# Optimization experiments

Hardware: AMD Instinct MI355X
Metric: run time of the kernel (lower is better)

The kernel has to match this reference:

```python
import jax, jax.numpy as jnp
import numpy as np

N_NODES = 20000
N_EDGES = 320000
EMB = 128


def setup_inputs() -> dict:
    key = jax.random.key(0)
    ks = jax.random.split(key, 8)
    h = jax.random.normal(ks[0], (N_NODES, EMB), dtype=jnp.float32)
    W1 = jax.random.normal(ks[1], (2 * EMB, 4 * EMB), dtype=jnp.float32) / np.sqrt(2 * EMB)
    b1 = jnp.zeros((4 * EMB,), dtype=jnp.float32)
    W2 = jax.random.normal(ks[2], (4 * EMB, 1), dtype=jnp.float32) / np.sqrt(4 * EMB)
    b2 = jnp.zeros((1,), dtype=jnp.float32)
    # logistic-noise uniforms for RelaxedBernoulli rsample, kept away from {0,1}
    u = jax.random.uniform(ks[3], (N_EDGES,), dtype=jnp.float32, minval=1e-6, maxval=1.0 - 1e-6)
    row = jax.random.randint(ks[4], (N_EDGES,), 0, N_NODES, dtype=jnp.int32)
    col = jax.random.randint(ks[5], (N_EDGES,), 0, N_NODES, dtype=jnp.int32)
    edge_mask = -jnp.ones((N_EDGES,), dtype=jnp.int32)  # torch code initializes mask to -1
    return {"h": h, "W1": W1, "b1": b1, "W2": W2, "b2": b2,
            "u": u, "row": row, "col": col, "edge_mask": edge_mask, "hierarchy": 0}


def _segment_softmax(scores, seg, num_segments):
    m = jax.ops.segment_max(scores, seg, num_segments=num_segments)
    e = jnp.exp(scores - m[seg])
    s = jax.ops.segment_sum(e, seg, num_segments=num_segments)
    return e / s[seg]


TEMPERATURE = 1.0
RATIO = 0.5  # threshold for hard bernoulli


def reference(h, W1, b1, W2, b2, u, row, col, edge_mask, hierarchy):
    # edge gather + concat: [E, 2*EMB]
    edge_rep = jnp.concatenate([h[row], h[col]], axis=-1)
    # 2-layer MLP edge scorer -> [E]
    hid = jax.nn.relu(edge_rep @ W1 + b1)
    scores = (hid @ W2 + b2).reshape(-1)
    # segment softmax over edges grouped by source node (torch: softmax(edge_score, edge_index[0]))
    probs = _segment_softmax(scores, row, N_NODES)
    # RelaxedBernoulli(temperature, probs).rsample(): sigmoid((logits + logistic)/T)
    logits = jnp.log(probs) - jnp.log1p(-probs)
    logistic = jnp.log(u) - jnp.log1p(-u)
    y = jax.nn.sigmoid((logits + logistic) / TEMPERATURE)
    y_hard = (y > RATIO).astype(y.dtype)
    y_st = jax.lax.stop_gradient(y_hard - y) + y  # straight-through
    # edge_mask[y == 1] = hierarchy + 1
    new_mask = jnp.where(y_st == 1.0, jnp.int32(hierarchy + 1), edge_mask)
    c_idx = new_mask > 0
    s_idx = new_mask == -1
    causal_w = jnp.where(c_idx, scores, 0.0)
    spu_w = jnp.where(s_idx, -scores, 0.0)
    return scores, y_st, new_mask, causal_w, spu_w
```

## Files before the change

### kernel.cpp

```cpp
#include <hip/hip_runtime.h>
#include <math.h>

#define N_NODES 20000
#define N_EDGES 320000
#define EMB 128
#define HID 512
#define NCHUNK ((N_NODES + 1023) / 1024)

#define RPW 4
#define WPB 2
#define RPB (RPW * WPB)
#define FE_BLOCKS ((N_NODES + RPB - 1) / RPB)

#define GEMM_MT ((N_NODES + 127) / 128)
#define GEMM_MFMA_BLOCKS (GEMM_MT * 8)
#define HIST_BLOCKS ((N_EDGES + 255) / 256)
#define GH_BLOCKS (GEMM_MFMA_BLOCKS + HIST_BLOCKS)
#define N_HTILES (N_NODES / 16)

#define PREP_H_BLOCKS 2500
#define PREP_W_BLOCKS 512
#define PREP_BLOCKS (PREP_H_BLOCKS + PREP_W_BLOCKS)

typedef __attribute__((ext_vector_type(8))) short bf16x8;
typedef __attribute__((ext_vector_type(4))) float f32x4;

#define MFMA16(a, b, c) __builtin_amdgcn_mfma_f32_16x16x32_bf16((a), (b), (c), 0, 0, 0)

__global__ void init_deg(int* __restrict__ deg, int* __restrict__ offs) {
    int i = blockIdx.x * 256 + threadIdx.x;
    if (i < N_NODES) deg[i] = 0;
    if (i == 0) offs[N_NODES] = N_EDGES;
}

__device__ __forceinline__ unsigned short bf16rn(float x) {
    unsigned u = __builtin_bit_cast(unsigned, x);
    u += 0x7FFFu + ((u >> 16) & 1u);
    return (unsigned short)(u >> 16);
}
__device__ __forceinline__ float bf2f(unsigned short b) {
    unsigned u = ((unsigned)b) << 16;
    return __builtin_bit_cast(float, u);
}
__device__ __forceinline__ void split3(float x, unsigned short& s1,
                                       unsigned short& s2, unsigned short& s3) {
    s1 = bf16rn(x);
    float r = x - bf2f(s1);
    s2 = bf16rn(r);
    float r2 = r - bf2f(s2);
    s3 = bf16rn(r2);
}

__global__ __launch_bounds__(256) void prep_pack(
    const float* __restrict__ h, const float* __restrict__ W1,
    unsigned short* __restrict__ hp1, unsigned short* __restrict__ hp2,
    unsigned short* __restrict__ hp3,
    unsigned short* __restrict__ wp1, unsigned short* __restrict__ wp2,
    unsigned short* __restrict__ wp3)
{
    const int bid = blockIdx.x, tid = threadIdx.x;

    if (bid < PREP_H_BLOCKS) {
        const int i4 = bid * 256 + tid;
        const float4 v = ((const float4*)h)[i4];
        const int r  = i4 >> 5;
        const int k0 = (i4 & 31) << 2;
        const int t = r >> 4, rowi = r & 15;
        const int ks = k0 >> 5;
        const int ln = (((k0 >> 3) & 3) << 4) + rowi;
        const int j0 = k0 & 7;
        const size_t off = (size_t)((t * 4 + ks) * 512) + ln * 8 + j0;
        unsigned short a1[4], a2[4], a3[4];
        split3(v.x, a1[0], a2[0], a3[0]);
        split3(v.y, a1[1], a2[1], a3[1]);
        split3(v.z, a1[2], a2[2], a3[2]);
        split3(v.w, a1[3], a2[3], a3[3]);
#define PACK4(dst, a) { \
            uint2 pk; \
            pk.x = (unsigned)a[0] | ((unsigned)a[1] << 16); \
            pk.y = (unsigned)a[2] | ((unsigned)a[3] << 16); \
            *(uint2*)((dst) + off) = pk; }
        PACK4(hp1, a1); PACK4(hp2, a2); PACK4(hp3, a3);
#undef PACK4
        return;
    }

    const int t = (bid - PREP_H_BLOCKS) * 256 + tid;
    const int n = t & 1023, k = t >> 10;
    const float x = W1[(size_t)(((n >> 9) << 7) + k) * HID + (n & 511)];
    unsigned short s1, s2, s3;
    split3(x, s1, s2, s3);
    const int tn = n >> 4, rown = n & 15;
    const int ks = k >> 5;
    const int ln = (((k >> 3) & 3) << 4) + rown;
    const int j = k & 7;
    const size_t off = (size_t)((tn * 4 + ks) * 512) + ln * 8 + j;
    wp1[off] = s1; wp2[off] = s2; wp3[off] = s3;
}

__global__ __launch_bounds__(256) void gemm_mfma(
    const unsigned short* __restrict__ hp1, const unsigned short* __restrict__ hp2,
    const unsigned short* __restrict__ hp3,
    const unsigned short* __restrict__ wp1, const unsigned short* __restrict__ wp2,
    const unsigned short* __restrict__ wp3,
    const float* __restrict__ b1, float* __restrict__ P, float* __restrict__ Q,
    const int* __restrict__ row, int* __restrict__ deg)
{
    const int bid = blockIdx.x;
    const int tid = threadIdx.x;

    if (bid >= GEMM_MFMA_BLOCKS) {
        const int e = (bid - GEMM_MFMA_BLOCKS) * 256 + tid;
        if (e < N_EDGES) atomicAdd(&deg[row[e]], 1);
        return;
    }

    const int nt = bid & 7, mt = bid >> 3;
    const int lane = tid & 63, w = tid >> 6;
    const int wm = w >> 1, wn = w & 1;
    const int l15 = lane & 15, l4 = lane >> 4;

    int tA[4];
#pragma unroll
    for (int i = 0; i < 4; ++i) {
        int t = mt * 8 + wm * 4 + i;
        tA[i] = (t < N_HTILES) ? t : N_HTILES - 1;
    }
    const int tB0 = nt * 8 + wn * 4;

    f32x4 acc[4][4];
#pragma unroll
    for (int i = 0; i < 4; ++i)
#pragma unroll
        for (int j = 0; j < 4; ++j) acc[i][j] = (f32x4){0.f, 0.f, 0.f, 0.f};

    const size_t lo = (size_t)lane * 8;

#pragma unroll
    for (int ks = 0; ks < 4; ++ks) {
        bf16x8 A1[4], A2[4], A3[4];
#pragma unroll
        for (int i = 0; i < 4; ++i) {
            const size_t ao = (size_t)((tA[i] * 4 + ks) * 512) + lo;
            A1[i] = *(const bf16x8*)(hp1 + ao);
            A2[i] = *(const bf16x8*)(hp2 + ao);
            A3[i] = *(const bf16x8*)(hp3 + ao);
        }
        const size_t b_base = (size_t)((tB0 * 4 + ks) * 512) + lo;
        bf16x8 Ba1 = *(const bf16x8*)(wp1 + b_base);
        bf16x8 Ba2 = *(const bf16x8*)(wp2 + b_base);
        bf16x8 Ba3 = *(const bf16x8*)(wp3 + b_base);
#pragma unroll
        for (int jn = 0; jn < 4; ++jn) {
            bf16x8 Bn1, Bn2, Bn3;
            if (jn < 3) {
                const size_t bo = b_base + (size_t)(jn + 1) * 2048;
                Bn1 = *(const bf16x8*)(wp1 + bo);
                Bn2 = *(const bf16x8*)(wp2 + bo);
                Bn3 = *(const bf16x8*)(wp3 + bo);
            }
#pragma unroll
            for (int i = 0; i < 4; ++i) {
                acc[i][jn] = MFMA16(A1[i], Ba1, acc[i][jn]);
                acc[i][jn] = MFMA16(A1[i], Ba2, acc[i][jn]);
                acc[i][jn] = MFMA16(A2[i], Ba1, acc[i][jn]);
                acc[i][jn] = MFMA16(A2[i], Ba2, acc[i][jn]);
                acc[i][jn] = MFMA16(A1[i], Ba3, acc[i][jn]);
                acc[i][jn] = MFMA16(A3[i], Ba1, acc[i][jn]);
            }
            if (jn < 3) { Ba1 = Bn1; Ba2 = Bn2; Ba3 = Bn3; }
        }
    }

    const int rbase = mt * 128 + wm * 64 + l4 * 4;
#pragma unroll
    for (int jn = 0; jn < 4; ++jn) {
        const int n = nt * 128 + wn * 64 + jn * 16 + l15;
        const bool isP = n < 512;
        float* __restrict__ dst = isP ? P : Q;
        const int col = n & 511;
        const float bias = isP ? b1[col] : 0.0f;
#pragma unroll
        for (int i = 0; i < 4; ++i) {
            const int rr0 = rbase + i * 16;
#pragma unroll
            for (int r = 0; r < 4; ++r) {
                const int rr = rr0 + r;
                if (rr < N_NODES)
                    dst[(size_t)rr * HID + col] = acc[i][jn][r] + bias;
            }
        }
    }
}

__device__ __forceinline__ int wave_incl_scan(int v, int lane) {
#pragma unroll
    for (int off = 1; off < 64; off <<= 1) {
        int t = __shfl_up(v, off, 64);
        if (lane >= off) v += t;
    }
    return v;
}

__global__ __launch_bounds__(1024) void scan_part(const int* __restrict__ deg,
                                                  int* __restrict__ part,
                                                  int* __restrict__ totals) {
    __shared__ int wsum[16];
    const int tid = threadIdx.x, lane = tid & 63, w = tid >> 6;
    const int i = blockIdx.x * 1024 + tid;
    int v = (i < N_NODES) ? deg[i] : 0;
    int incl = wave_incl_scan(v, lane);
    if (lane == 63) wsum[w] = incl;
    __syncthreads();
    if (w == 0) {
        int x = (lane < 16) ? wsum[lane] : 0;
        int xs = wave_incl_scan(x, lane);
        if (lane < 16) wsum[lane] = xs - x;
        if (lane == 15) totals[blockIdx.x] = xs;
    }
    __syncthreads();
    if (i < N_NODES) part[i] = wsum[w] + incl - v;
}

__global__ __launch_bounds__(1024) void scan_apply(const int* __restrict__ part,
                                                   const int* __restrict__ totals,
                                                   int* __restrict__ cursor,
                                                   int* __restrict__ offs) {
    __shared__ int carry_s;
    const int tid = threadIdx.x;
    if (tid < 64) {
        int v = (tid < NCHUNK) ? totals[tid] : 0;
        int incl = wave_incl_scan(v, tid);
        if (tid == (int)blockIdx.x) carry_s = incl - v;
    }
    __syncthreads();
    const int i = blockIdx.x * 1024 + tid;
    if (i < N_NODES) {
        int o = part[i] + carry_s;
        cursor[i] = o;
        offs[i] = o;
    }
}

__global__ void scatter_edges(const int* __restrict__ row, const int* __restrict__ col,
                              int* __restrict__ cursor,
                              unsigned short* __restrict__ cols16,
                              int* __restrict__ inv) {
    int e = blockIdx.x * 256 + threadIdx.x;
    if (e >= N_EDGES) return;
    int r = row[e];
    int pos = atomicAdd(&cursor[r], 1);
    cols16[pos] = (unsigned short)col[e];
    inv[e] = pos;
}

__device__ __forceinline__ float dot8_relu(const float4 qa, const float4 qb,
                                           const float4 p0, const float4 p1,
                                           const float4 w0, const float4 w1) {
    float t = 0.0f;
    t = fmaf(fmaxf(p0.x + qa.x, 0.0f), w0.x, t);
    t = fmaf(fmaxf(p0.y + qa.y, 0.0f), w0.y, t);
    t = fmaf(fmaxf(p0.z + qa.z, 0.0f), w0.z, t);
    t = fmaf(fmaxf(p0.w + qa.w, 0.0f), w0.w, t);
    t = fmaf(fmaxf(p1.x + qb.x, 0.0f), w1.x, t);
    t = fmaf(fmaxf(p1.y + qb.y, 0.0f), w1.y, t);
    t = fmaf(fmaxf(p1.z + qb.z, 0.0f), w1.z, t);
    t = fmaf(fmaxf(p1.w + qb.w, 0.0f), w1.w, t);
    return t;
}

__device__ __forceinline__ float chunk_scores(
    const float* __restrict__ Q, const unsigned short* __restrict__ cols16,
    int es_base, int nch, int lane, int j0,
    const float4 p0, const float4 p1, const float4 w0, const float4 w1,
    float bias2)
{
    int mycol = 0;
    if (lane < nch) mycol = (int)cols16[es_base + lane];
    float mysc = -INFINITY;

#define QL2(k, bb, d0, d1) { \
        int c_ = __shfl(mycol, (bb) + (k), 64); \
        const float* __restrict__ q_ = Q + (size_t)c_ * HID; \
        d0 = *(const float4*)(q_ + j0); \
        d1 = *(const float4*)(q_ + 256 + j0); }

    float4 a00, a01, a10, a11;
    QL2(0, 0, a00, a01); QL2(1, 0, a10, a11);

    for (int b = 0; b < nch; b += 2) {
        float4 n00, n01, n10, n11;
        const bool more = (b + 2) < nch;
        if (more) { QL2(0, b + 2, n00, n01); QL2(1, b + 2, n10, n11); }

        float s0 = dot8_relu(a00, a01, p0, p1, w0, w1);
        float s1 = dot8_relu(a10, a11, p0, p1, w0, w1);

#pragma unroll
        for (int off = 32; off > 0; off >>= 1) {
            s0 += __shfl_xor(s0, off, 64);
            s1 += __shfl_xor(s1, off, 64);
        }

        const int k = lane - b;
        if ((unsigned)k < 2u && lane < nch) mysc = (k ? s1 : s0) + bias2;

        if (more) { a00 = n00; a01 = n01; a10 = n10; a11 = n11; }
    }
#undef QL2
    return mysc;
}

__global__ __launch_bounds__(128) void fused_edge(
    const float* __restrict__ P, const float* __restrict__ Q,
    const float* __restrict__ W2, const float* __restrict__ b2,
    const unsigned short* __restrict__ cols16, const int* __restrict__ offs,
    float2* __restrict__ tmp)
{
    const int tid = threadIdx.x, lane = tid & 63, w = tid >> 6;
    const int r0 = blockIdx.x * RPB + w * RPW;
    const int r1 = (r0 + RPW < N_NODES) ? r0 + RPW : N_NODES;
    const int j0 = lane << 2;

    const float4 w0 = *(const float4*)(W2 + j0);
    const float4 w1 = *(const float4*)(W2 + 256 + j0);
    const float bias2 = b2[0];

    for (int r = r0; r < r1; ++r) {
        const int es = offs[r], ee = offs[r + 1];
        const int d = ee - es;
        if (d == 0) continue;

        const float* __restrict__ prow = P + (size_t)r * HID;
        const float4 p0 = *(const float4*)(prow + j0);
        const float4 p1 = *(const float4*)(prow + 256 + j0);

        if (d <= 64) {
            float mysc = chunk_scores(Q, cols16, es, d, lane, j0,
                                      p0, p1, w0, w1, bias2);

            float m = mysc;
#pragma unroll
            for (int off = 32; off > 0; off >>= 1)
                m = fmaxf(m, __shfl_xor(m, off, 64));

            float ev = (lane < d) ? expf(mysc - m) : 0.0f;
            float ssum = ev;
#pragma unroll
            for (int off = 32; off > 0; off >>= 1)
                ssum += __shfl_xor(ssum, off, 64);

            if (lane < d) {
                float p = ev / ssum;
                float logits = logf(p) - log1pf(-p);
                tmp[es + lane] = make_float2(mysc, logits);
            }
        } else {
            for (int base = 0; base < d; base += 64) {
                const int nch = (d - base < 64) ? d - base : 64;
                float mysc = chunk_scores(Q, cols16, es + base, nch, lane, j0,
                                          p0, p1, w0, w1, bias2);
                if (lane < nch) tmp[es + base + lane].x = mysc;
            }

            float m = -INFINITY;
            for (int j = lane; j < d; j += 64)
                m = fmaxf(m, tmp[es + j].x);
#pragma unroll
            for (int off = 32; off > 0; off >>= 1)
                m = fmaxf(m, __shfl_xor(m, off, 64));

            float ssum = 0.0f;
            for (int j = lane; j < d; j += 64)
                ssum += expf(tmp[es + j].x - m);
#pragma unroll
            for (int off = 32; off > 0; off >>= 1)
                ssum += __shfl_xor(ssum, off, 64);

            for (int j = lane; j < d; j += 64) {
                float s = tmp[es + j].x;
                float p = expf(s - m) / ssum;
                float logits = logf(p) - log1pf(-p);
                tmp[es + j] = make_float2(s, logits);
            }
        }
    }
}

__global__ __launch_bounds__(256) void unperm(
    const float2* __restrict__ tmp, const int* __restrict__ inv,
    const float* __restrict__ u, const int* __restrict__ edge_mask,
    const int* __restrict__ hierarchy,
    float* __restrict__ scores, float* __restrict__ out_y,
    float* __restrict__ out_mask, float* __restrict__ out_causal,
    float* __restrict__ out_spu)
{
    const int e = blockIdx.x * 256 + threadIdx.x;
    if (e >= N_EDGES) return;
    const float2 t = tmp[inv[e]];
    const float s = t.x;
    const float uu = u[e];
    const float L = logf(uu) - log1pf(-uu);
    const float y = 1.0f / (1.0f + expf(-(t.y + L)));
    const bool hard = y > 0.5f;
    const int mm = hard ? (hierarchy[0] + 1) : edge_mask[e];
    scores[e]     = s;
    out_y[e]      = hard ? 1.0f : 0.0f;
    out_mask[e]   = (float)mm;
    out_causal[e] = (mm > 0)   ?  s : 0.0f;
    out_spu[e]    = (mm == -1) ? -s : 0.0f;
}

extern "C" void kernel_launch(void* const* d_in, const int* in_sizes, int n_in,
                              void* d_out, int out_size, void* d_ws, size_t ws_size,
                              hipStream_t stream) {
    const float* h_ptr = (const float*)d_in[0];
    const float* W1    = (const float*)d_in[1];
    const float* b1    = (const float*)d_in[2];
    const float* W2    = (const float*)d_in[3];
    const float* b2    = (const float*)d_in[4];
    const float* u     = (const float*)d_in[5];
    const int*   row   = (const int*)d_in[6];
    const int*   col   = (const int*)d_in[7];
    const int*   emask = (const int*)d_in[8];
    const int*   hier  = (const int*)d_in[9];

    float* out        = (float*)d_out;
    float* scores     = out;
    float* out_y      = out + (size_t)N_EDGES;
    float* out_mask   = out + 2 * (size_t)N_EDGES;
    float* out_causal = out + 3 * (size_t)N_EDGES;
    float* out_spu    = out + 4 * (size_t)N_EDGES;

    float*          P      = (float*)d_ws;
    float*          Qm     = P + (size_t)N_NODES * HID;
    unsigned short* hp1    = (unsigned short*)(Qm + (size_t)N_NODES * HID);
    unsigned short* hp2    = hp1 + (size_t)N_NODES * EMB;
    unsigned short* hp3    = hp2 + (size_t)N_NODES * EMB;
    unsigned short* wp1    = hp3 + (size_t)N_NODES * EMB;
    unsigned short* wp2    = wp1 + 1024 * 128;
    unsigned short* wp3    = wp2 + 1024 * 128;
    int*            deg    = (int*)(wp3 + 1024 * 128);
    int*            cursor = deg + N_NODES;
    int*            offs   = cursor + N_NODES;
    int*            part   = offs + N_NODES + 1;
    int*            totals = part + N_NODES;
    float2*         tmp    = (float2*)hp1;
    unsigned short* cols16 = (unsigned short*)(tmp + N_EDGES);
    int*            inv    = (int*)(cols16 + N_EDGES);

    hipLaunchKernelGGL(init_deg, dim3((N_NODES + 255) / 256), dim3(256), 0, stream,
                       deg, offs);

    hipLaunchKernelGGL(prep_pack, dim3(PREP_BLOCKS), dim3(256), 0, stream,
                       h_ptr, W1, hp1, hp2, hp3, wp1, wp2, wp3);

    hipLaunchKernelGGL(gemm_mfma, dim3(GH_BLOCKS), dim3(256), 0, stream,
                       hp1, hp2, hp3, wp1, wp2, wp3, b1, P, Qm, row, deg);

    hipLaunchKernelGGL(scan_part, dim3(NCHUNK), dim3(1024), 0, stream, deg, part, totals);
    hipLaunchKernelGGL(scan_apply, dim3(NCHUNK), dim3(1024), 0, stream,
                       part, totals, cursor, offs);
    hipLaunchKernelGGL(scatter_edges, dim3((N_EDGES + 255) / 256), dim3(256), 0, stream,
                       row, col, cursor, cols16, inv);

    hipLaunchKernelGGL(fused_edge, dim3(FE_BLOCKS), dim3(128), 0, stream,
                       P, Qm, W2, b2, cols16, offs, tmp);

    hipLaunchKernelGGL(unperm, dim3((N_EDGES + 255) / 256), dim3(256), 0, stream,
                       tmp, inv, u, emask, hier,
                       scores, out_y, out_mask, out_causal, out_spu);
}
```

Measured before the change: 279.3 us.

## Retile node GEMM with LDS-staged weights and fold deg init into prep

Moves the node-level GEMM to 256x64 tiles. Each block stages its 64-column slice of the three bf16 weight splits into shared memory with global_load_lds, and each wave owns 64 rows and prefetches the next k-slice of A into registers. The weight packing now has each thread write 8 bf16 values per store instead of scalar stores, and the deg/offs initialisation is merged into prep_pack, which removes one launch. The trade-off is more blocks and repeated A loads across the 16 column tiles, in exchange for less global B traffic, plus an occupancy hint of 2 blocks per CU.

```diff
diff --git a/kernel.cpp b/kernel.cpp
--- a/kernel.cpp
+++ b/kernel.cpp
@@ -12,25 +12,27 @@
 #define RPB (RPW * WPB)
 #define FE_BLOCKS ((N_NODES + RPB - 1) / RPB)
 
-#define GEMM_MT ((N_NODES + 127) / 128)
-#define GEMM_MFMA_BLOCKS (GEMM_MT * 8)
+#define GEMM_MT ((N_NODES + 255) / 256)
+#define GEMM_NT 16
+#define GEMM_MFMA_BLOCKS (GEMM_MT * GEMM_NT)
 #define HIST_BLOCKS ((N_EDGES + 255) / 256)
 #define GH_BLOCKS (GEMM_MFMA_BLOCKS + HIST_BLOCKS)
 #define N_HTILES (N_NODES / 16)
 
 #define PREP_H_BLOCKS 2500
-#define PREP_W_BLOCKS 512
-#define PREP_BLOCKS (PREP_H_BLOCKS + PREP_W_BLOCKS)
+#define PREP_W_BLOCKS 64
+#define PREP_Z_BLOCKS ((N_NODES + 255) / 256)
+#define PREP_BLOCKS (PREP_H_BLOCKS + PREP_W_BLOCKS + PREP_Z_BLOCKS)
 
 typedef __attribute__((ext_vector_type(8))) short bf16x8;
 typedef __attribute__((ext_vector_type(4))) float f32x4;
 
 #define MFMA16(a, b, c) __builtin_amdgcn_mfma_f32_16x16x32_bf16((a), (b), (c), 0, 0, 0)
 
-__global__ void init_deg(int* __restrict__ deg, int* __restrict__ offs) {
-    int i = blockIdx.x * 256 + threadIdx.x;
-    if (i < N_NODES) deg[i] = 0;
-    if (i == 0) offs[N_NODES] = N_EDGES;
+__device__ __forceinline__ void stage16(const unsigned short* g, unsigned short* l) {
+    __builtin_amdgcn_global_load_lds(
+        (const __attribute__((address_space(1))) void*)g,
+        (__attribute__((address_space(3))) void*)l, 16, 0, 0);
 }
 
 __device__ __forceinline__ unsigned short bf16rn(float x) {
@@ -56,7 +58,8 @@
     unsigned short* __restrict__ hp1, unsigned short* __restrict__ hp2,
     unsigned short* __restrict__ hp3,
     unsigned short* __restrict__ wp1, unsigned short* __restrict__ wp2,
-    unsigned short* __restrict__ wp3)
+    unsigned short* __restrict__ wp3,
+    int* __restrict__ deg, int* __restrict__ offs)
 {
     const int bid = blockIdx.x, tid = threadIdx.x;
 
@@ -85,20 +88,40 @@
         return;
     }
 
-    const int t = (bid - PREP_H_BLOCKS) * 256 + tid;
-    const int n = t & 1023, k = t >> 10;
-    const float x = W1[(size_t)(((n >> 9) << 7) + k) * HID + (n & 511)];
-    unsigned short s1, s2, s3;
-    split3(x, s1, s2, s3);
-    const int tn = n >> 4, rown = n & 15;
-    const int ks = k >> 5;
-    const int ln = (((k >> 3) & 3) << 4) + rown;
-    const int j = k & 7;
-    const size_t off = (size_t)((tn * 4 + ks) * 512) + ln * 8 + j;
-    wp1[off] = s1; wp2[off] = s2; wp3[off] = s3;
-}
-
-__global__ __launch_bounds__(256) void gemm_mfma(
+    if (bid < PREP_H_BLOCKS + PREP_W_BLOCKS) {
+        const int t = (bid - PREP_H_BLOCKS) * 256 + tid;
+        const int n = t & 1023, kg = t >> 10;
+        const int k0 = kg << 3;
+        const int wrow0 = ((n >> 9) << 7) + k0;
+        const int wcol  = n & 511;
+        unsigned short s1[8], s2[8], s3[8];
+#pragma unroll
+        for (int j = 0; j < 8; ++j) {
+            const float x = W1[(size_t)(wrow0 + j) * HID + wcol];
+            split3(x, s1[j], s2[j], s3[j]);
+        }
+        const int tn = n >> 4, rown = n & 15;
+        const int ks = k0 >> 5;
+        const int ln = (((k0 >> 3) & 3) << 4) + rown;
+        const size_t off = (size_t)((tn * 4 + ks) * 512) + ln * 8;
+#define PACK8(dst, a) { \
+            uint4 pk; \
+            pk.x = (unsigned)a[0] | ((unsigned)a[1] << 16); \
+            pk.y = (unsigned)a[2] | ((unsigned)a[3] << 16); \
+            pk.z = (unsigned)a[4] | ((unsigned)a[5] << 16); \
+            pk.w = (unsigned)a[6] | ((unsigned)a[7] << 16); \
+            *(uint4*)((dst) + off) = pk; }
+        PACK8(wp1, s1); PACK8(wp2, s2); PACK8(wp3, s3);
+#undef PACK8
+        return;
+    }
+
+    const int i = (bid - PREP_H_BLOCKS - PREP_W_BLOCKS) * 256 + tid;
+    if (i < N_NODES) deg[i] = 0;
+    if (i == 0) offs[N_NODES] = N_EDGES;
+}
+
+__global__ __launch_bounds__(256, 2) void gemm_mfma(
     const unsigned short* __restrict__ hp1, const unsigned short* __restrict__ hp2,
     const unsigned short* __restrict__ hp3,
     const unsigned short* __restrict__ wp1, const unsigned short* __restrict__ wp2,
@@ -115,18 +138,44 @@
         return;
     }
 
-    const int nt = bid & 7, mt = bid >> 3;
+    __shared__ unsigned short bs[4][4][3][512];
+
+    const int mt = bid >> 4, nt = bid & 15;
     const int lane = tid & 63, w = tid >> 6;
-    const int wm = w >> 1, wn = w & 1;
     const int l15 = lane & 15, l4 = lane >> 4;
 
+    {
+        const int tn = nt * 4 + w;
+        const unsigned short* wps0 = wp1;
+        const unsigned short* wps1 = wp2;
+        const unsigned short* wps2 = wp3;
+#pragma unroll
+        for (int ks = 0; ks < 4; ++ks) {
+            const size_t so = (size_t)((tn * 4 + ks) * 512) + lane * 8;
+            stage16(wps0 + so, &bs[w][ks][0][0]);
+            stage16(wps1 + so, &bs[w][ks][1][0]);
+            stage16(wps2 + so, &bs[w][ks][2][0]);
+        }
+    }
+
     int tA[4];
 #pragma unroll
     for (int i = 0; i < 4; ++i) {
-        int t = mt * 8 + wm * 4 + i;
+        int t = mt * 16 + w * 4 + i;
         tA[i] = (t < N_HTILES) ? t : N_HTILES - 1;
     }
-    const int tB0 = nt * 8 + wn * 4;
+    size_t aoff[4];
+#pragma unroll
+    for (int i = 0; i < 4; ++i)
+        aoff[i] = (size_t)(tA[i] * 4) * 512 + lane * 8;
+
+    bf16x8 A1[4], A2[4], A3[4];
+#pragma unroll
+    for (int i = 0; i < 4; ++i) {
+        A1[i] = *(const bf16x8*)(hp1 + aoff[i]);
+        A2[i] = *(const bf16x8*)(hp2 + aoff[i]);
+        A3[i] = *(const bf16x8*)(hp3 + aoff[i]);
+    }
 
     f32x4 acc[4][4];
 #pragma unroll
@@ -134,31 +183,26 @@
 #pragma unroll
         for (int j = 0; j < 4; ++j) acc[i][j] = (f32x4){0.f, 0.f, 0.f, 0.f};
 
-    const size_t lo = (size_t)lane * 8;
+    __syncthreads();
 
 #pragma unroll
     for (int ks = 0; ks < 4; ++ks) {
-        bf16x8 A1[4], A2[4], A3[4];
-#pragma unroll
-        for (int i = 0; i < 4; ++i) {
-            const size_t ao = (size_t)((tA[i] * 4 + ks) * 512) + lo;
-            A1[i] = *(const bf16x8*)(hp1 + ao);
-            A2[i] = *(const bf16x8*)(hp2 + ao);
-            A3[i] = *(const bf16x8*)(hp3 + ao);
-        }
-        const size_t b_base = (size_t)((tB0 * 4 + ks) * 512) + lo;
-        bf16x8 Ba1 = *(const bf16x8*)(wp1 + b_base);
-        bf16x8 Ba2 = *(const bf16x8*)(wp2 + b_base);
-        bf16x8 Ba3 = *(const bf16x8*)(wp3 + b_base);
+        bf16x8 N1[4], N2[4], N3[4];
+        if (ks < 3) {
+            const size_t ko = (size_t)(ks + 1) * 512;
+#pragma unroll
+            for (int i = 0; i < 4; ++i) {
+                N1[i] = *(const bf16x8*)(hp1 + aoff[i] + ko);
+                N2[i] = *(const bf16x8*)(hp2 + aoff[i] + ko);
+                N3[i] = *(const bf16x8*)(hp3 + aoff[i] + ko);
+            }
+        }
 #pragma unroll
         for (int jn = 0; jn < 4; ++jn) {
-            bf16x8 Bn1, Bn2, Bn3;
-            if (jn < 3) {
-                const size_t bo = b_base + (size_t)(jn + 1) * 2048;
-                Bn1 = *(const bf16x8*)(wp1 + bo);
-                Bn2 = *(const bf16x8*)(wp2 + bo);
-                Bn3 = *(const bf16x8*)(wp3 + bo);
-            }
+            const unsigned short* bb = &bs[jn][ks][0][0] + lane * 8;
+            const bf16x8 Ba1 = *(const bf16x8*)(bb);
+            const bf16x8 Ba2 = *(const bf16x8*)(bb + 512);
+            const bf16x8 Ba3 = *(const bf16x8*)(bb + 1024);
 #pragma unroll
             for (int i = 0; i < 4; ++i) {
                 acc[i][jn] = MFMA16(A1[i], Ba1, acc[i][jn]);
@@ -168,21 +212,26 @@
                 acc[i][jn] = MFMA16(A1[i], Ba3, acc[i][jn]);
                 acc[i][jn] = MFMA16(A3[i], Ba1, acc[i][jn]);
             }
-            if (jn < 3) { Ba1 = Bn1; Ba2 = Bn2; Ba3 = Bn3; }
-        }
-    }
-
-    const int rbase = mt * 128 + wm * 64 + l4 * 4;
+        }
+        if (ks < 3) {
+#pragma unroll
+            for (int i = 0; i < 4; ++i) {
+                A1[i] = N1[i]; A2[i] = N2[i]; A3[i] = N3[i];
+            }
+        }
+    }
+
+    const int rb0 = mt * 256 + w * 64;
 #pragma unroll
     for (int jn = 0; jn < 4; ++jn) {
-        const int n = nt * 128 + wn * 64 + jn * 16 + l15;
+        const int n = nt * 64 + jn * 16 + l15;
         const bool isP = n < 512;
         float* __restrict__ dst = isP ? P : Q;
         const int col = n & 511;
         const float bias = isP ? b1[col] : 0.0f;
 #pragma unroll
         for (int i = 0; i < 4; ++i) {
-            const int rr0 = rbase + i * 16;
+            const int rr0 = rb0 + i * 16 + l4 * 4;
 #pragma unroll
             for (int r = 0; r < 4; ++r) {
                 const int rr = rr0 + r;
@@ -449,11 +498,8 @@
     unsigned short* cols16 = (unsigned short*)(tmp + N_EDGES);
     int*            inv    = (int*)(cols16 + N_EDGES);
 
-    hipLaunchKernelGGL(init_deg, dim3((N_NODES + 255) / 256), dim3(256), 0, stream,
-                       deg, offs);
-
     hipLaunchKernelGGL(prep_pack, dim3(PREP_BLOCKS), dim3(256), 0, stream,
-                       h_ptr, W1, hp1, hp2, hp3, wp1, wp2, wp3);
+                       h_ptr, W1, hp1, hp2, hp3, wp1, wp2, wp3, deg, offs);
 
     hipLaunchKernelGGL(gemm_mfma, dim3(GH_BLOCKS), dim3(256), 0, stream,
                        hp1, hp2, hp3, wp1, wp2, wp3, b1, P, Qm, row, deg);
```

Result: faster. 262.3 us (-6.1%).
